# Optimization experiments

Measured on AMD Instinct MI355X. Metric: run time of the kernel, lower is better.

Reference implementation:

```python
import jax, jax.numpy as jnp
import numpy as np

# Event marker constants (PASS/MAP both trigger map writes, STEP triggers step writes)
PASS, MAP, STEP = 0, 1, 2
GRAPH_STEPS = 3
B, T, D, K, V = 64, 12, 256, 256, 512
S = 2 * K  # num_symbols


def gelu(x):
    return jax.nn.gelu(x, approximate=False)  # torch nn.GELU default = exact erf


def mlp2(x, W1, b1, W2, b2):
    return gelu(x @ W1 + b1) @ W2 + b2


def setup_inputs() -> dict:
    key = jax.random.key(0)
    ks = jax.random.split(key, 32)

    def lin(k, fan_in, shape):
        return (jax.random.normal(k, shape, dtype=jnp.float32) / np.float32(np.sqrt(fan_in)))

    return {
        "event_marker": jax.random.randint(ks[0], (B, T), 0, 3),
        "source_idx": jax.random.randint(ks[1], (B, T), 0, S),
        "source_valid": jax.random.randint(ks[2], (B, T), 0, 2),
        "target_symbol_idx": jax.random.randint(ks[3], (B, T), 0, S),
        "target_symbol_valid": jax.random.randint(ks[4], (B, T), 0, 2),
        "target_value_idx": jax.random.randint(ks[5], (B, T), 0, V),
        "target_value_valid": jax.random.randint(ks[6], (B, T), 0, 2),
        "query_idx": jax.random.randint(ks[7], (B,), 0, S),
        "query_valid": jax.random.randint(ks[8], (B,), 0, 2),
        "evidence": jax.random.normal(ks[9], (B, T, D), dtype=jnp.float32),
        "symbol_emb": jax.random.normal(ks[10], (S, D), dtype=jnp.float32) * 0.02,
        "value_emb": jax.random.normal(ks[11], (V, D), dtype=jnp.float32) * 0.02,
        "Wmg1": lin(ks[12], D, (D, D)), "bmg1": jnp.zeros((D,), jnp.float32),
        "Wmg2": lin(ks[13], D, (D, 1)), "bmg2": jnp.zeros((1,), jnp.float32),
        "Wsg1": lin(ks[14], D, (D, D)), "bsg1": jnp.zeros((D,), jnp.float32),
        "Wsg2": lin(ks[15], D, (D, 1)), "bsg2": jnp.zeros((1,), jnp.float32),
        "Wf1": lin(ks[16], 2 * D, (2 * D, D)), "bf1": jnp.zeros((D,), jnp.float32),
        "Wf2": lin(ks[17], D, (D, D)), "bf2": jnp.zeros((D,), jnp.float32),
        "Wo1": lin(ks[18], 2 * D, (2 * D, D)), "bo1": jnp.zeros((D,), jnp.float32),
        "Wo2": lin(ks[19], D, (D, V)), "bo2": jnp.zeros((V,), jnp.float32),
    }


def reference(event_marker, source_idx, source_valid, target_symbol_idx,
              target_symbol_valid, target_value_idx, target_value_valid,
              query_idx, query_valid, evidence, symbol_emb, value_emb,
              Wmg1, bmg1, Wmg2, bmg2, Wsg1, bsg1, Wsg2, bsg2,
              Wf1, bf1, Wf2, bf2, Wo1, bo1, Wo2, bo2):
    f32 = evidence.dtype
    brange = jnp.arange(B)

    # --- TypedGraphMemory.update, applied over T sequential events ---
    # one-hot outer-product write  ==  scatter-add of gated scalar at (b, src, tgt)
    def step(carry, ev):
        map_mem, step_mem = carry
        marker, src, sv, tsym, tsv, tval, tvv, evd = ev
        mg = jax.nn.sigmoid(mlp2(evd, Wmg1, bmg1, Wmg2, bmg2))[:, 0]  # [B]
        sg = jax.nn.sigmoid(mlp2(evd, Wsg1, bsg1, Wsg2, bsg2))[:, 0]  # [B]
        map_mask = (((marker == PASS) | (marker == MAP)) & (sv > 0) & (tvv > 0)).astype(f32)
        step_mask = ((marker == STEP) & (sv > 0) & (tsv > 0)).astype(f32)
        src_c = jnp.clip(src, 0, S - 1)
        tsym_c = jnp.clip(tsym, 0, S - 1)
        tval_c = jnp.clip(tval, 0, V - 1)
        map_mem = map_mem.at[brange, src_c, tval_c].add(mg * map_mask)
        step_mem = step_mem.at[brange, src_c, tsym_c].add(sg * step_mask)
        return (map_mem, step_mem), None

    ev_seq = (event_marker.T, source_idx.T, source_valid.T, target_symbol_idx.T,
              target_symbol_valid.T, target_value_idx.T, target_value_valid.T,
              jnp.swapaxes(evidence, 0, 1))  # time-major
    init = (jnp.zeros((B, S, V), f32), jnp.zeros((B, S, S), f32))
    (map_mem, step_mem), _ = jax.lax.scan(step, init, ev_seq)

    # --- TypedGraphMemory.query_readout ---
    walk = jax.nn.one_hot(jnp.clip(query_idx, 0, S - 1), S, dtype=f32)
    walk = walk * query_valid.astype(f32)[:, None]
    acc_v = jnp.einsum('bs,bsv->bv', walk, map_mem)   # [B,V]
    acc_s = walk @ symbol_emb                         # [B,D]
    for _ in range(GRAPH_STEPS):
        walk = jnp.einsum('bs,bst->bt', walk, step_mem)
        acc_v = acc_v + jnp.einsum('bs,bsv->bv', walk, map_mem)
        acc_s = acc_s + walk @ symbol_emb
    graph_state = jnp.concatenate([acc_s, acc_v @ value_emb], axis=-1)  # [B,2D]
    logits = mlp2(graph_state, Wo1, bo1, Wo2, bo2)      # [B,V]
    feedback = mlp2(graph_state, Wf1, bf1, Wf2, bf2)    # [B,D]
    return logits, feedback
```

## Files before the change

kernel.cpp:

```cpp
#include <hip/hip_runtime.h>
#include <math.h>

#define NB 64
#define NT 12
#define ND 256
#define NS 512
#define NV 512

__device__ float g_gates[2 * NB * NT];
__device__ float g_gs[NB * 512];
__device__ float g_H[2 * NB * 256];

__device__ __forceinline__ float gelu_exact(float x) {
    return 0.5f * x * (1.0f + erff(x * 0.70710678118654752f));
}
__device__ __forceinline__ float sigmoidf_(float x) {
    return 1.0f / (1.0f + __expf(-x));
}

__global__ __launch_bounds__(1024) void k_gates(
    const float* __restrict__ evidence,
    const float* __restrict__ Wmg1, const float* __restrict__ bmg1,
    const float* __restrict__ Wmg2, const float* __restrict__ bmg2,
    const float* __restrict__ Wsg1, const float* __restrict__ bsg1,
    const float* __restrict__ Wsg2, const float* __restrict__ bsg2)
{
    const int blk = blockIdx.x;
    const int b  = blk >> 2;
    const int g  = (blk >> 1) & 1;
    const int th = blk & 1;
    const int t0 = th * 6;
    const int tid = threadIdx.x;
    const int j = tid & 255;
    const int ih = tid >> 8;
    const int lane = tid & 63, wv = tid >> 6;

    __shared__ float part[3][6][256];
    __shared__ float red[4][6];

    const float* __restrict__ W1 = g ? Wsg1 : Wmg1;
    const float* __restrict__ b1 = g ? bsg1 : bmg1;
    const float* __restrict__ W2 = g ? Wsg2 : Wmg2;
    const float* __restrict__ b2 = g ? bsg2 : bmg2;
    const float* __restrict__ ev = evidence + b * (NT * ND) + t0 * ND;

    float h[6];
    #pragma unroll
    for (int t = 0; t < 6; ++t) h[t] = 0.0f;

    const int ibase = ih * 64;
    #pragma unroll 8
    for (int ii = 0; ii < 64; ++ii) {
        const int i = ibase + ii;
        float w = W1[i * ND + j];
        #pragma unroll
        for (int t = 0; t < 6; ++t) h[t] += ev[t * ND + i] * w;
    }

    if (ih > 0) {
        #pragma unroll
        for (int t = 0; t < 6; ++t) part[ih - 1][t][j] = h[t];
    }
    __syncthreads();
    if (ih == 0) {
        const float b1j = b1[j], w2j = W2[j];
        #pragma unroll
        for (int t = 0; t < 6; ++t) {
            float v = gelu_exact(h[t] + part[0][t][j] + part[1][t][j] +
                                 part[2][t][j] + b1j) * w2j;
            #pragma unroll
            for (int off = 32; off > 0; off >>= 1) v += __shfl_down(v, off, 64);
            if (lane == 0) red[wv][t] = v;
        }
    }
    __syncthreads();
    if (tid < 6) {
        float s = red[0][tid] + red[1][tid] + red[2][tid] + red[3][tid] + b2[0];
        g_gates[g * (NB * NT) + b * NT + t0 + tid] = sigmoidf_(s);
    }
}

__global__ __launch_bounds__(512) void k_readout(
    const int* __restrict__ marker, const int* __restrict__ srci,
    const int* __restrict__ srcv, const int* __restrict__ tsymi,
    const int* __restrict__ tsymv, const int* __restrict__ tvali,
    const int* __restrict__ tvalv, const int* __restrict__ qidx,
    const int* __restrict__ qvld,
    const float* __restrict__ symbol_emb, const float* __restrict__ value_emb)
{
    const int b = blockIdx.x, tid = threadIdx.x;
    __shared__ float walk[NS], nxt[NS];
    __shared__ int   esrc[NT], etsym[NT], etval[NT];
    __shared__ float mapw[NT], stepw[NT];
    __shared__ int   sidx[64]; __shared__ float sval[64];
    __shared__ int   vidx[64]; __shared__ float vval[64];
    __shared__ int   scnt, vcnt;

    walk[tid] = 0.f; nxt[tid] = 0.f;
    if (tid == 0) { scnt = 0; vcnt = 0; }
    if (tid < NT) {
        int e = b * NT + tid;
        int mk = marker[e];
        int sv_ = srcv[e], tsv_ = tsymv[e], tvv_ = tvalv[e];
        esrc[tid]  = min(max(srci[e], 0), NS - 1);
        etsym[tid] = min(max(tsymi[e], 0), NS - 1);
        etval[tid] = min(max(tvali[e], 0), NV - 1);
        bool mmask = ((mk == 0) || (mk == 1)) && (sv_ > 0) && (tvv_ > 0);
        bool smask = (mk == 2) && (sv_ > 0) && (tsv_ > 0);
        mapw[tid]  = mmask ? g_gates[0 * (NB * NT) + e] : 0.f;
        stepw[tid] = smask ? g_gates[1 * (NB * NT) + e] : 0.f;
    }
    __syncthreads();
    if (tid == 0) {
        int qc = min(max(qidx[b], 0), NS - 1);
        float qv = (float)qvld[b];
        walk[qc] = qv;
        if (qv != 0.f) { sidx[0] = qc; sval[0] = qv; scnt = 1; }
    }
    __syncthreads();
    if (tid < NT) {
        float c = walk[esrc[tid]] * mapw[tid];
        if (c != 0.f) { int k = atomicAdd(&vcnt, 1); vidx[k] = etval[tid]; vval[k] = c; }
    }
    __syncthreads();
    for (int stp = 0; stp < 3; ++stp) {
        if (tid < NT) {
            float c = walk[esrc[tid]] * stepw[tid];
            if (c != 0.f) {
                atomicAdd(&nxt[etsym[tid]], c);
                int k = atomicAdd(&scnt, 1); sidx[k] = etsym[tid]; sval[k] = c;
            }
        }
        __syncthreads();
        { float a = nxt[tid]; walk[tid] = a; nxt[tid] = 0.f; }
        __syncthreads();
        if (tid < NT) {
            float c = walk[esrc[tid]] * mapw[tid];
            if (c != 0.f) { int k = atomicAdd(&vcnt, 1); vidx[k] = etval[tid]; vval[k] = c; }
        }
        __syncthreads();
    }
    const int d = tid & 255;
    const float* __restrict__ emb  = (tid < 256) ? symbol_emb : value_emb;
    const int*   idxl = (tid < 256) ? sidx : vidx;
    const float* vall = (tid < 256) ? sval : vval;
    const int n = (tid < 256) ? scnt : vcnt;
    float acc = 0.f;
    int k = 0;
    for (; k + 4 <= n; k += 4) {
        int   i0 = idxl[k],     i1 = idxl[k + 1], i2 = idxl[k + 2], i3 = idxl[k + 3];
        float w0 = vall[k],     w1 = vall[k + 1], w2 = vall[k + 2], w3 = vall[k + 3];
        float r0 = emb[i0 * ND + d], r1 = emb[i1 * ND + d];
        float r2 = emb[i2 * ND + d], r3 = emb[i3 * ND + d];
        acc += w0 * r0; acc += w1 * r1; acc += w2 * r2; acc += w3 * r3;
    }
    for (; k < n; ++k) acc += vall[k] * emb[idxl[k] * ND + d];
    g_gs[b * 512 + (tid < 256 ? 0 : 256) + d] = acc;
}

__global__ __launch_bounds__(512) void k_mlp1(
    const float* __restrict__ Wo1, const float* __restrict__ bo1,
    const float* __restrict__ Wf1, const float* __restrict__ bf1)
{
    const int blk = blockIdx.x;
    const int m  = blk >> 7;
    const int r  = blk & 127;
    const int js = r >> 5;
    const int bp = r & 31;
    const int tid = threadIdx.x;
    const int lane = tid & 63;
    const int oct = tid >> 6;
    const int j = js * 64 + lane;
    const int b0 = bp * 2, b1_ = b0 + 1;

    const float* __restrict__ W1 = m ? Wf1 : Wo1;
    const float* __restrict__ x0 = g_gs + b0 * 512;
    const float* __restrict__ x1 = g_gs + b1_ * 512;

    float a0 = 0.f, a1 = 0.f;
    const int i0 = oct * 64;
    #pragma unroll 8
    for (int ii = 0; ii < 64; ++ii) {
        const int i = i0 + ii;
        float w = W1[i * 256 + j];
        a0 += x0[i] * w; a1 += x1[i] * w;
    }
    __shared__ float2 part[8][64];
    part[oct][lane] = make_float2(a0, a1);
    __syncthreads();
    if (oct == 0) {
        const float* __restrict__ bias = m ? bf1 : bo1;
        float bj = bias[j];
        float s0 = 0.f, s1 = 0.f;
        #pragma unroll
        for (int q = 0; q < 8; ++q) {
            float2 p = part[q][lane];
            s0 += p.x; s1 += p.y;
        }
        g_H[m * (NB * 256) + b0 * 256 + j]  = gelu_exact(s0 + bj);
        g_H[m * (NB * 256) + b1_ * 256 + j] = gelu_exact(s1 + bj);
    }
}

__global__ __launch_bounds__(512) void k_mlp2(
    const float* __restrict__ Wo2, const float* __restrict__ bo2,
    const float* __restrict__ Wf2, const float* __restrict__ bf2,
    float* __restrict__ out)
{
    const int blk = blockIdx.x;
    const int tid = threadIdx.x;
    const int lane = tid & 63;
    const int oct = tid >> 6;
    __shared__ float4 part[8][64];

    if (blk < 128) {
        const int vs = blk >> 4, bt = blk & 15;
        const int v = vs * 64 + lane;
        const int bb = bt * 4;
        const float* __restrict__ h0 = g_H + (bb + 0) * 256;
        const float* __restrict__ h1 = g_H + (bb + 1) * 256;
        const float* __restrict__ h2 = g_H + (bb + 2) * 256;
        const float* __restrict__ h3 = g_H + (bb + 3) * 256;
        float a0 = 0.f, a1 = 0.f, a2 = 0.f, a3 = 0.f;
        const int k0 = oct * 32;
        #pragma unroll 8
        for (int kk = 0; kk < 32; ++kk) {
            const int k = k0 + kk;
            float w = Wo2[k * 512 + v];
            a0 += h0[k] * w; a1 += h1[k] * w; a2 += h2[k] * w; a3 += h3[k] * w;
        }
        part[oct][lane] = make_float4(a0, a1, a2, a3);
        __syncthreads();
        if (oct == 0) {
            float bv = bo2[v];
            float s0 = 0.f, s1 = 0.f, s2 = 0.f, s3 = 0.f;
            #pragma unroll
            for (int q = 0; q < 8; ++q) {
                float4 p = part[q][lane];
                s0 += p.x; s1 += p.y; s2 += p.z; s3 += p.w;
            }
            out[(bb + 0) * 512 + v] = s0 + bv;
            out[(bb + 1) * 512 + v] = s1 + bv;
            out[(bb + 2) * 512 + v] = s2 + bv;
            out[(bb + 3) * 512 + v] = s3 + bv;
        }
    } else {
        const int r = blk - 128;
        const int ds = r >> 4, bt = r & 15;
        const int d = ds * 64 + lane;
        const int bb = bt * 4;
        const float* __restrict__ h0 = g_H + (NB * 256) + (bb + 0) * 256;
        const float* __restrict__ h1 = g_H + (NB * 256) + (bb + 1) * 256;
        const float* __restrict__ h2 = g_H + (NB * 256) + (bb + 2) * 256;
        const float* __restrict__ h3 = g_H + (NB * 256) + (bb + 3) * 256;
        float a0 = 0.f, a1 = 0.f, a2 = 0.f, a3 = 0.f;
        const int k0 = oct * 32;
        #pragma unroll 8
        for (int kk = 0; kk < 32; ++kk) {
            const int k = k0 + kk;
            float w = Wf2[k * 256 + d];
            a0 += h0[k] * w; a1 += h1[k] * w; a2 += h2[k] * w; a3 += h3[k] * w;
        }
        part[oct][lane] = make_float4(a0, a1, a2, a3);
        __syncthreads();
        if (oct == 0) {
            float bd = bf2[d];
            float s0 = 0.f, s1 = 0.f, s2 = 0.f, s3 = 0.f;
            #pragma unroll
            for (int q = 0; q < 8; ++q) {
                float4 p = part[q][lane];
                s0 += p.x; s1 += p.y; s2 += p.z; s3 += p.w;
            }
            out[NB * NV + (bb + 0) * 256 + d] = s0 + bd;
            out[NB * NV + (bb + 1) * 256 + d] = s1 + bd;
            out[NB * NV + (bb + 2) * 256 + d] = s2 + bd;
            out[NB * NV + (bb + 3) * 256 + d] = s3 + bd;
        }
    }
}

extern "C" void kernel_launch(void* const* d_in, const int* in_sizes, int n_in,
                              void* d_out, int out_size, void* d_ws, size_t ws_size,
                              hipStream_t stream) {
    const int* event_marker       = (const int*)d_in[0];
    const int* source_idx         = (const int*)d_in[1];
    const int* source_valid       = (const int*)d_in[2];
    const int* target_symbol_idx  = (const int*)d_in[3];
    const int* target_symbol_vld  = (const int*)d_in[4];
    const int* target_value_idx   = (const int*)d_in[5];
    const int* target_value_vld   = (const int*)d_in[6];
    const int* query_idx          = (const int*)d_in[7];
    const int* query_valid        = (const int*)d_in[8];
    const float* evidence   = (const float*)d_in[9];
    const float* symbol_emb = (const float*)d_in[10];
    const float* value_emb  = (const float*)d_in[11];
    const float* Wmg1 = (const float*)d_in[12]; const float* bmg1 = (const float*)d_in[13];
    const float* Wmg2 = (const float*)d_in[14]; const float* bmg2 = (const float*)d_in[15];
    const float* Wsg1 = (const float*)d_in[16]; const float* bsg1 = (const float*)d_in[17];
    const float* Wsg2 = (const float*)d_in[18]; const float* bsg2 = (const float*)d_in[19];
    const float* Wf1  = (const float*)d_in[20]; const float* bf1  = (const float*)d_in[21];
    const float* Wf2  = (const float*)d_in[22]; const float* bf2  = (const float*)d_in[23];
    const float* Wo1  = (const float*)d_in[24]; const float* bo1  = (const float*)d_in[25];
    const float* Wo2  = (const float*)d_in[26]; const float* bo2  = (const float*)d_in[27];

    (void)d_ws; (void)ws_size;

    k_gates<<<dim3(256), dim3(1024), 0, stream>>>(
        evidence, Wmg1, bmg1, Wmg2, bmg2, Wsg1, bsg1, Wsg2, bsg2);
    k_readout<<<dim3(64), dim3(512), 0, stream>>>(
        event_marker, source_idx, source_valid, target_symbol_idx,
        target_symbol_vld, target_value_idx, target_value_vld,
        query_idx, query_valid, symbol_emb, value_emb);
    k_mlp1<<<dim3(256), dim3(512), 0, stream>>>(Wo1, bo1, Wf1, bf1);
    k_mlp2<<<dim3(192), dim3(512), 0, stream>>>(Wo2, bo2, Wf2, bf2, (float*)d_out);
}
```

Measured before the change: 140.6 us.

## Fuse graph readout into first MLP layer and vectorize gate evidence loads

Merges the readout kernel into the first MLP kernel. Each of the 256 blocks recomputes the graph walk and embedding gathers for its two batch rows and keeps the graph state in shared memory, which removes one launch and the global round trip through g_gs. The cost is redundant readout work: each batch row is recomputed by 8 blocks. Separately, the gate kernel now loads evidence as float4 and unrolls by four input rows to cut load instruction count.

```diff
diff --git a/kernel.cpp b/kernel.cpp
--- a/kernel.cpp
+++ b/kernel.cpp
@@ -8,7 +8,6 @@
 #define NV 512
 
 __device__ float g_gates[2 * NB * NT];
-__device__ float g_gs[NB * 512];
 __device__ float g_H[2 * NB * 256];
 
 __device__ __forceinline__ float gelu_exact(float x) {
@@ -49,12 +48,25 @@
     for (int t = 0; t < 6; ++t) h[t] = 0.0f;
 
     const int ibase = ih * 64;
-    #pragma unroll 8
-    for (int ii = 0; ii < 64; ++ii) {
+    #pragma unroll 4
+    for (int ii = 0; ii < 64; ii += 4) {
         const int i = ibase + ii;
-        float w = W1[i * ND + j];
-        #pragma unroll
-        for (int t = 0; t < 6; ++t) h[t] += ev[t * ND + i] * w;
+        float4 e0 = *reinterpret_cast<const float4*>(ev + 0 * ND + i);
+        float4 e1 = *reinterpret_cast<const float4*>(ev + 1 * ND + i);
+        float4 e2 = *reinterpret_cast<const float4*>(ev + 2 * ND + i);
+        float4 e3 = *reinterpret_cast<const float4*>(ev + 3 * ND + i);
+        float4 e4 = *reinterpret_cast<const float4*>(ev + 4 * ND + i);
+        float4 e5 = *reinterpret_cast<const float4*>(ev + 5 * ND + i);
+        float w0 = W1[(i + 0) * ND + j];
+        float w1 = W1[(i + 1) * ND + j];
+        float w2 = W1[(i + 2) * ND + j];
+        float w3 = W1[(i + 3) * ND + j];
+        h[0] += e0.x * w0; h[0] += e0.y * w1; h[0] += e0.z * w2; h[0] += e0.w * w3;
+        h[1] += e1.x * w0; h[1] += e1.y * w1; h[1] += e1.z * w2; h[1] += e1.w * w3;
+        h[2] += e2.x * w0; h[2] += e2.y * w1; h[2] += e2.z * w2; h[2] += e2.w * w3;
+        h[3] += e3.x * w0; h[3] += e3.y * w1; h[3] += e3.z * w2; h[3] += e3.w * w3;
+        h[4] += e4.x * w0; h[4] += e4.y * w1; h[4] += e4.z * w2; h[4] += e4.w * w3;
+        h[5] += e5.x * w0; h[5] += e5.y * w1; h[5] += e5.z * w2; h[5] += e5.w * w3;
     }
 
     if (ih > 0) {
@@ -80,85 +92,13 @@
     }
 }
 
-__global__ __launch_bounds__(512) void k_readout(
+__global__ __launch_bounds__(512) void k_ro_mlp1(
     const int* __restrict__ marker, const int* __restrict__ srci,
     const int* __restrict__ srcv, const int* __restrict__ tsymi,
     const int* __restrict__ tsymv, const int* __restrict__ tvali,
     const int* __restrict__ tvalv, const int* __restrict__ qidx,
     const int* __restrict__ qvld,
-    const float* __restrict__ symbol_emb, const float* __restrict__ value_emb)
-{
-    const int b = blockIdx.x, tid = threadIdx.x;
-    __shared__ float walk[NS], nxt[NS];
-    __shared__ int   esrc[NT], etsym[NT], etval[NT];
-    __shared__ float mapw[NT], stepw[NT];
-    __shared__ int   sidx[64]; __shared__ float sval[64];
-    __shared__ int   vidx[64]; __shared__ float vval[64];
-    __shared__ int   scnt, vcnt;
-
-    walk[tid] = 0.f; nxt[tid] = 0.f;
-    if (tid == 0) { scnt = 0; vcnt = 0; }
-    if (tid < NT) {
-        int e = b * NT + tid;
-        int mk = marker[e];
-        int sv_ = srcv[e], tsv_ = tsymv[e], tvv_ = tvalv[e];
-        esrc[tid]  = min(max(srci[e], 0), NS - 1);
-        etsym[tid] = min(max(tsymi[e], 0), NS - 1);
-        etval[tid] = min(max(tvali[e], 0), NV - 1);
-        bool mmask = ((mk == 0) || (mk == 1)) && (sv_ > 0) && (tvv_ > 0);
-        bool smask = (mk == 2) && (sv_ > 0) && (tsv_ > 0);
-        mapw[tid]  = mmask ? g_gates[0 * (NB * NT) + e] : 0.f;
-        stepw[tid] = smask ? g_gates[1 * (NB * NT) + e] : 0.f;
-    }
-    __syncthreads();
-    if (tid == 0) {
-        int qc = min(max(qidx[b], 0), NS - 1);
-        float qv = (float)qvld[b];
-        walk[qc] = qv;
-        if (qv != 0.f) { sidx[0] = qc; sval[0] = qv; scnt = 1; }
-    }
-    __syncthreads();
-    if (tid < NT) {
-        float c = walk[esrc[tid]] * mapw[tid];
-        if (c != 0.f) { int k = atomicAdd(&vcnt, 1); vidx[k] = etval[tid]; vval[k] = c; }
-    }
-    __syncthreads();
-    for (int stp = 0; stp < 3; ++stp) {
-        if (tid < NT) {
-            float c = walk[esrc[tid]] * stepw[tid];
-            if (c != 0.f) {
-                atomicAdd(&nxt[etsym[tid]], c);
-                int k = atomicAdd(&scnt, 1); sidx[k] = etsym[tid]; sval[k] = c;
-            }
-        }
-        __syncthreads();
-        { float a = nxt[tid]; walk[tid] = a; nxt[tid] = 0.f; }
-        __syncthreads();
-        if (tid < NT) {
-            float c = walk[esrc[tid]] * mapw[tid];
-            if (c != 0.f) { int k = atomicAdd(&vcnt, 1); vidx[k] = etval[tid]; vval[k] = c; }
-        }
-        __syncthreads();
-    }
-    const int d = tid & 255;
-    const float* __restrict__ emb  = (tid < 256) ? symbol_emb : value_emb;
-    const int*   idxl = (tid < 256) ? sidx : vidx;
-    const float* vall = (tid < 256) ? sval : vval;
-    const int n = (tid < 256) ? scnt : vcnt;
-    float acc = 0.f;
-    int k = 0;
-    for (; k + 4 <= n; k += 4) {
-        int   i0 = idxl[k],     i1 = idxl[k + 1], i2 = idxl[k + 2], i3 = idxl[k + 3];
-        float w0 = vall[k],     w1 = vall[k + 1], w2 = vall[k + 2], w3 = vall[k + 3];
-        float r0 = emb[i0 * ND + d], r1 = emb[i1 * ND + d];
-        float r2 = emb[i2 * ND + d], r3 = emb[i3 * ND + d];
-        acc += w0 * r0; acc += w1 * r1; acc += w2 * r2; acc += w3 * r3;
-    }
-    for (; k < n; ++k) acc += vall[k] * emb[idxl[k] * ND + d];
-    g_gs[b * 512 + (tid < 256 ? 0 : 256) + d] = acc;
-}
-
-__global__ __launch_bounds__(512) void k_mlp1(
+    const float* __restrict__ symbol_emb, const float* __restrict__ value_emb,
     const float* __restrict__ Wo1, const float* __restrict__ bo1,
     const float* __restrict__ Wf1, const float* __restrict__ bf1)
 {
@@ -173,19 +113,116 @@
     const int j = js * 64 + lane;
     const int b0 = bp * 2, b1_ = b0 + 1;
 
+    __shared__ float walk2[2][NS], nxt2[2][NS];
+    __shared__ int   esrc2[2][NT], etsym2[2][NT], etval2[2][NT];
+    __shared__ float mapw2[2][NT], stepw2[2][NT];
+    __shared__ int   sidx2[2][64]; __shared__ float sval2[2][64];
+    __shared__ int   vidx2[2][64]; __shared__ float vval2[2][64];
+    __shared__ int   scnt2[2], vcnt2[2];
+    __shared__ float gs_l[2][512];
+    __shared__ float2 part[8][64];
+
+    walk2[0][tid] = 0.f; nxt2[0][tid] = 0.f;
+    walk2[1][tid] = 0.f; nxt2[1][tid] = 0.f;
+    if (tid < 2) { scnt2[tid] = 0; vcnt2[tid] = 0; }
+    if (tid < 2 * NT) {
+        const int u = (tid >= NT) ? 1 : 0;
+        const int tt = tid - u * NT;
+        const int b = u ? b1_ : b0;
+        const int e = b * NT + tt;
+        int mk = marker[e];
+        int sv_ = srcv[e], tsv_ = tsymv[e], tvv_ = tvalv[e];
+        esrc2[u][tt]  = min(max(srci[e], 0), NS - 1);
+        etsym2[u][tt] = min(max(tsymi[e], 0), NS - 1);
+        etval2[u][tt] = min(max(tvali[e], 0), NV - 1);
+        bool mmask = ((mk == 0) || (mk == 1)) && (sv_ > 0) && (tvv_ > 0);
+        bool smask = (mk == 2) && (sv_ > 0) && (tsv_ > 0);
+        mapw2[u][tt]  = mmask ? g_gates[0 * (NB * NT) + e] : 0.f;
+        stepw2[u][tt] = smask ? g_gates[1 * (NB * NT) + e] : 0.f;
+    }
+    __syncthreads();
+    if (tid < 2) {
+        const int u = tid;
+        const int b = u ? b1_ : b0;
+        int qc = min(max(qidx[b], 0), NS - 1);
+        float qv = (float)qvld[b];
+        walk2[u][qc] = qv;
+        if (qv != 0.f) { sidx2[u][0] = qc; sval2[u][0] = qv; scnt2[u] = 1; }
+    }
+    __syncthreads();
+    if (tid < 2 * NT) {
+        const int u = (tid >= NT) ? 1 : 0;
+        const int tt = tid - u * NT;
+        float c = walk2[u][esrc2[u][tt]] * mapw2[u][tt];
+        if (c != 0.f) { int k = atomicAdd(&vcnt2[u], 1); vidx2[u][k] = etval2[u][tt]; vval2[u][k] = c; }
+    }
+    __syncthreads();
+    for (int stp = 0; stp < 3; ++stp) {
+        if (tid < 2 * NT) {
+            const int u = (tid >= NT) ? 1 : 0;
+            const int tt = tid - u * NT;
+            float c = walk2[u][esrc2[u][tt]] * stepw2[u][tt];
+            if (c != 0.f) {
+                atomicAdd(&nxt2[u][etsym2[u][tt]], c);
+                int k = atomicAdd(&scnt2[u], 1); sidx2[u][k] = etsym2[u][tt]; sval2[u][k] = c;
+            }
+        }
+        __syncthreads();
+        { float a0 = nxt2[0][tid]; walk2[0][tid] = a0; nxt2[0][tid] = 0.f;
+          float a1 = nxt2[1][tid]; walk2[1][tid] = a1; nxt2[1][tid] = 0.f; }
+        __syncthreads();
+        if (tid < 2 * NT) {
+            const int u = (tid >= NT) ? 1 : 0;
+            const int tt = tid - u * NT;
+            float c = walk2[u][esrc2[u][tt]] * mapw2[u][tt];
+            if (c != 0.f) { int k = atomicAdd(&vcnt2[u], 1); vidx2[u][k] = etval2[u][tt]; vval2[u][k] = c; }
+        }
+        __syncthreads();
+    }
+    {
+        const int u = tid >> 8, d = tid & 255;
+        {
+            const int n = scnt2[u];
+            const int*   idxl = sidx2[u];
+            const float* vall = sval2[u];
+            float acc = 0.f; int k = 0;
+            for (; k + 4 <= n; k += 4) {
+                int   i0 = idxl[k],     i1 = idxl[k + 1], i2 = idxl[k + 2], i3 = idxl[k + 3];
+                float w0 = vall[k],     w1 = vall[k + 1], w2 = vall[k + 2], w3 = vall[k + 3];
+                float r0 = symbol_emb[i0 * ND + d], r1 = symbol_emb[i1 * ND + d];
+                float r2 = symbol_emb[i2 * ND + d], r3 = symbol_emb[i3 * ND + d];
+                acc += w0 * r0; acc += w1 * r1; acc += w2 * r2; acc += w3 * r3;
+            }
+            for (; k < n; ++k) acc += vall[k] * symbol_emb[idxl[k] * ND + d];
+            gs_l[u][d] = acc;
+        }
+        {
+            const int n = vcnt2[u];
+            const int*   idxl = vidx2[u];
+            const float* vall = vval2[u];
+            float acc = 0.f; int k = 0;
+            for (; k + 4 <= n; k += 4) {
+                int   i0 = idxl[k],     i1 = idxl[k + 1], i2 = idxl[k + 2], i3 = idxl[k + 3];
+                float w0 = vall[k],     w1 = vall[k + 1], w2 = vall[k + 2], w3 = vall[k + 3];
+                float r0 = value_emb[i0 * ND + d], r1 = value_emb[i1 * ND + d];
+                float r2 = value_emb[i2 * ND + d], r3 = value_emb[i3 * ND + d];
+                acc += w0 * r0; acc += w1 * r1; acc += w2 * r2; acc += w3 * r3;
+            }
+            for (; k < n; ++k) acc += vall[k] * value_emb[idxl[k] * ND + d];
+            gs_l[u][256 + d] = acc;
+        }
+    }
+    __syncthreads();
+
     const float* __restrict__ W1 = m ? Wf1 : Wo1;
-    const float* __restrict__ x0 = g_gs + b0 * 512;
-    const float* __restrict__ x1 = g_gs + b1_ * 512;
-
     float a0 = 0.f, a1 = 0.f;
     const int i0 = oct * 64;
     #pragma unroll 8
     for (int ii = 0; ii < 64; ++ii) {
         const int i = i0 + ii;
         float w = W1[i * 256 + j];
-        a0 += x0[i] * w; a1 += x1[i] * w;
-    }
-    __shared__ float2 part[8][64];
+        a0 += gs_l[0][i] * w; a1 += gs_l[1][i] * w;
+    }
     part[oct][lane] = make_float2(a0, a1);
     __syncthreads();
     if (oct == 0) {
@@ -307,10 +344,9 @@
 
     k_gates<<<dim3(256), dim3(1024), 0, stream>>>(
         evidence, Wmg1, bmg1, Wmg2, bmg2, Wsg1, bsg1, Wsg2, bsg2);
-    k_readout<<<dim3(64), dim3(512), 0, stream>>>(
+    k_ro_mlp1<<<dim3(256), dim3(512), 0, stream>>>(
         event_marker, source_idx, source_valid, target_symbol_idx,
         target_symbol_vld, target_value_idx, target_value_vld,
-        query_idx, query_valid, symbol_emb, value_emb);
-    k_mlp1<<<dim3(256), dim3(512), 0, stream>>>(Wo1, bo1, Wf1, bf1);
+        query_idx, query_valid, symbol_emb, value_emb, Wo1, bo1, Wf1, bf1);
     k_mlp2<<<dim3(192), dim3(512), 0, stream>>>(Wo2, bo2, Wf2, bf2, (float*)d_out);
 }
```

After: 139.5 us. No clear change (-0.8%).
